# Optimization experiments

Hardware: AMD Instinct MI355X
Metric: run time of the kernel (lower is better)

Reference implementation:

```python
import jax, jax.numpy as jnp
import numpy as np

N_STATE = 16
PNAMES = ['in_w', 'conv_w', 'conv_b', 'xproj_w', 'dt_w', 'dt_b', 'A_log', 'D', 'ln_g', 'ln_b', 'out_w']


def _ss2d_params(key, dm, K):
    di = 2 * dm                       # expand = 2
    dr = (dm + 15) // 16              # dt_rank = ceil(d_model/16)
    ks = jax.random.split(key, 6)
    s = lambda k, shape, sc: jax.random.normal(k, shape, jnp.float32) * sc
    cshape = (di, 1, 3, 3) if K == 4 else (di, 1, 3)   # depthwise conv kernel
    return {
        'in_w': s(ks[0], (2 * di, dm), dm ** -0.5),
        'conv_w': s(ks[1], cshape, 0.3),
        'conv_b': jnp.zeros((di,), jnp.float32),
        'xproj_w': s(ks[2], (K, dr + 2 * N_STATE, di), di ** -0.5),
        'dt_w': s(ks[3], (K, di, dr), dr ** -0.5),
        'dt_b': s(ks[4], (K, di), 0.1),
        'A_log': jnp.log(jnp.arange(1, N_STATE + 1, dtype=jnp.float32)) * jnp.ones((K, di, N_STATE), jnp.float32),
        'D': jnp.ones((K, di), jnp.float32),
        'ln_g': jnp.ones((di,), jnp.float32),
        'ln_b': jnp.zeros((di,), jnp.float32),
        'out_w': s(ks[5], (dm, di), di ** -0.5),
    }


def _ln(x, g, b, eps=1e-5):
    m = jnp.mean(x, -1, keepdims=True)
    v = jnp.mean((x - m) ** 2, -1, keepdims=True)
    return (x - m) * jax.lax.rsqrt(v + eps) * g + b


def _scan_branches(xs, p):
    # xs: (B, K, di, L) -- selective scan along L for each direction k
    dr = p['dt_w'].shape[-1]
    x_dbl = jnp.einsum('bkdl,kcd->bkcl', xs, p['xproj_w'])
    dts, Bs, Cs = jnp.split(x_dbl, [dr, dr + N_STATE], axis=2)
    delta = jax.nn.softplus(jnp.einsum('bkrl,kdr->bkdl', dts, p['dt_w']) + p['dt_b'][None, :, :, None])
    A = -jnp.exp(p['A_log'])                               # (K, di, N)
    dA = jnp.exp(jnp.einsum('bkdl,kdn->lbkdn', delta, A))  # time-major for scan
    dBu = jnp.einsum('bkdl,bknl,bkdl->lbkdn', delta, Bs, xs)

    def step(h, io):
        a, bu = io
        h = a * h + bu
        return h, h

    h0 = jnp.zeros(dA.shape[1:], xs.dtype)
    _, hs = jax.lax.scan(step, h0, (dA, dBu))              # (L, B, K, di, N)
    y = jnp.einsum('lbkdn,bknl->bkdl', hs, Cs)
    return y + xs * p['D'][None, :, :, None]


def _ss2d_2d(x, p):
    # VMamba SS2D: x (B, H, W, dm) -> (B, H, W, dm), 4 scan directions
    xz = jnp.einsum('bhwc,ec->bhwe', x, p['in_w'])
    xin, z = jnp.split(xz, 2, -1)
    u = xin.transpose(0, 3, 1, 2)
    u = jax.lax.conv_general_dilated(u, p['conv_w'], (1, 1), 'SAME',
        dimension_numbers=('NCHW', 'OIHW', 'NCHW'), feature_group_count=u.shape[1])
    u = jax.nn.silu(u + p['conv_b'][None, :, None, None])
    Bb, di, H, W = u.shape
    L = H * W
    xf = u.reshape(Bb, di, L)                              # row-major
    xt = u.transpose(0, 1, 3, 2).reshape(Bb, di, L)        # col-major
    xs = jnp.stack([xf, xt, xf[..., ::-1], xt[..., ::-1]], 1)
    ys = _scan_branches(xs, p)                             # (B, 4, di, L)
    y0 = ys[:, 0]
    y2 = ys[:, 2][..., ::-1]
    y1 = ys[:, 1].reshape(Bb, di, W, H).transpose(0, 1, 3, 2).reshape(Bb, di, L)
    y3 = ys[:, 3][..., ::-1].reshape(Bb, di, W, H).transpose(0, 1, 3, 2).reshape(Bb, di, L)
    y = (y0 + y1 + y2 + y3).transpose(0, 2, 1).reshape(Bb, H, W, di)
    y = _ln(y, p['ln_g'], p['ln_b']) * jax.nn.silu(z)
    return jnp.einsum('bhwe,ce->bhwc', y, p['out_w'])


def _ss2d_1d(x, p):
    # SS2D_xb fuse block: x (B, L, dm) -> (B, L, dm), bidirectional 1D scan
    xz = jnp.einsum('blc,ec->ble', x, p['in_w'])
    xin, z = jnp.split(xz, 2, -1)
    u = xin.transpose(0, 2, 1)
    u = jax.lax.conv_general_dilated(u, p['conv_w'], (1,), 'SAME',
        dimension_numbers=('NCH', 'OIH', 'NCH'), feature_group_count=u.shape[1])
    u = jax.nn.silu(u + p['conv_b'][None, :, None])
    xs = jnp.stack([u, u[..., ::-1]], 1)                   # K = 2
    ys = _scan_branches(xs, p)
    y = (ys[:, 0] + ys[:, 1][..., ::-1]).transpose(0, 2, 1)
    y = _ln(y, p['ln_g'], p['ln_b']) * jax.nn.silu(z)
    return jnp.einsum('ble,ce->blc', y, p['out_w'])


def _bridge(C1, C2, C3, p1, p2, p3, pf, n1_g, n1_b):
    y1 = _ss2d_2d(C1.transpose(0, 2, 3, 1), p1).transpose(0, 3, 1, 2)
    y2 = _ss2d_2d(C2.transpose(0, 2, 3, 1), p2).transpose(0, 3, 1, 2)
    y3 = _ss2d_2d(C3.transpose(0, 2, 3, 1), p3).transpose(0, 3, 1, 2)
    B_, C, H, W = y1.shape                                 # C=24, H=W=112
    # faithful RAW reshapes (no permute), exactly as the torch source does
    F1 = y1.reshape(B_, H * W, C)
    F2 = y2.reshape(B_, H * W // 2, C)
    F3 = y3.reshape(B_, H * W // 4, C)
    F = jnp.concatenate([F1, F2, F3], axis=1)              # (B, 21952, 24)
    F = F + _ss2d_1d(_ln(F, n1_g, n1_b), pf)               # dropout = identity (eval)
    o1 = F[:, :12544, :].reshape(B_, C, H, W)
    o2 = F[:, 12544:18816, :].reshape(B_, C * 2, H // 2, W // 2)
    o3 = F[:, 18816:, :].reshape(B_, C * 4, H // 4, W // 4)
    return (o1, o2, o3)


def setup_inputs() -> dict:
    key = jax.random.key(0)
    ks = jax.random.split(key, 7)
    inp = {
        'C1': jax.random.normal(ks[0], (1, 24, 112, 112), jnp.float32),
        'C2': jax.random.normal(ks[1], (1, 48, 56, 56), jnp.float32),
        'C3': jax.random.normal(ks[2], (1, 96, 28, 28), jnp.float32),
    }
    for pfx, dm, K, kk in [('m1', 24, 4, ks[3]), ('m2', 48, 4, ks[4]), ('m3', 96, 4, ks[5]), ('fz', 24, 2, ks[6])]:
        p = _ss2d_params(kk, dm, K)
        for n in PNAMES:
            inp[pfx + '_' + n] = p[n]
    inp['n1_g'] = jnp.ones((24,), jnp.float32)
    inp['n1_b'] = jnp.zeros((24,), jnp.float32)
    return inp


def reference(C1, C2, C3, m1_in_w, m1_conv_w, m1_conv_b, m1_xproj_w, m1_dt_w, m1_dt_b, m1_A_log, m1_D, m1_ln_g, m1_ln_b, m1_out_w, m2_in_w, m2_conv_w, m2_conv_b, m2_xproj_w, m2_dt_w, m2_dt_b, m2_A_log, m2_D, m2_ln_g, m2_ln_b, m2_out_w, m3_in_w, m3_conv_w, m3_conv_b, m3_xproj_w, m3_dt_w, m3_dt_b, m3_A_log, m3_D, m3_ln_g, m3_ln_b, m3_out_w, fz_in_w, fz_conv_w, fz_conv_b, fz_xproj_w, fz_dt_w, fz_dt_b, fz_A_log, fz_D, fz_ln_g, fz_ln_b, fz_out_w, n1_g, n1_b):
    p1 = dict(zip(PNAMES, (m1_in_w, m1_conv_w, m1_conv_b, m1_xproj_w, m1_dt_w, m1_dt_b, m1_A_log, m1_D, m1_ln_g, m1_ln_b, m1_out_w)))
    p2 = dict(zip(PNAMES, (m2_in_w, m2_conv_w, m2_conv_b, m2_xproj_w, m2_dt_w, m2_dt_b, m2_A_log, m2_D, m2_ln_g, m2_ln_b, m2_out_w)))
    p3 = dict(zip(PNAMES, (m3_in_w, m3_conv_w, m3_conv_b, m3_xproj_w, m3_dt_w, m3_dt_b, m3_A_log, m3_D, m3_ln_g, m3_ln_b, m3_out_w)))
    pf = dict(zip(PNAMES, (fz_in_w, fz_conv_w, fz_conv_b, fz_xproj_w, fz_dt_w, fz_dt_b, fz_A_log, fz_D, fz_ln_g, fz_ln_b, fz_out_w)))
    return _bridge(C1, C2, C3, p1, p2, p3, pf, n1_g, n1_b)
```

## Files before the change

kernel.cpp:

```cpp
#include <hip/hip_runtime.h>
#include <hip/hip_bf16.h>
#include <hip/hip_fp16.h>

#define NST 16
#define L2E 1.4426950408889634f

typedef const void* inp;
typedef __half h16;

struct Job {
  inp Cin;
  inp in_w, conv_w, conv_b, xproj_w, dt_w, dt_b, A_log, D, ln_g, ln_b, out_w;
  h16 *u_pre, *z, *u, *delta, *Bs, *Cs, *yg;
  h16 *Hc;
  float *yacc, *Wc, *bc, *Ssum, *A2t, *F0out;
  float *outF; const float* resid;
  const int* aflg;
  int dm, di, dr, K, H, W, L, NCH, CLEN, is2d, TL, CG, PT, cinf;
};
struct Jobs { Job j[4]; int n; const int* dtf; };

__device__ __forceinline__ float ldw(inp p, size_t i, int f32){
  return f32 ? ((const float*)p)[i]
             : __bfloat162float(((const __hip_bfloat16*)p)[i]);
}
__device__ __forceinline__ float hf(const h16* p, size_t i){ return __half2float(p[i]); }
__device__ __forceinline__ float sigm(float x){ return 1.0f/(1.0f + __expf(-x)); }
__device__ __forceinline__ float silu_(float x){ return x * sigm(x); }
__device__ __forceinline__ float softp(float x){ return (x > 20.0f) ? x : __logf(1.0f + __expf(x)); }

__device__ __forceinline__ int map_pos(const Job& J, int k, int l){
  int rev   = J.is2d ? (k >= 2) : (k == 1);
  int trans = J.is2d ? (k & 1) : 0;
  int sl = rev ? (J.L - 1 - l) : l;
  return trans ? ((sl % J.H)*J.W + sl / J.H) : sl;
}

union F4H { float4 f; __half2 h[4]; };

__device__ __forceinline__ void ld16v(const h16* p, float* o){
  const float4* q = (const float4*)p;
  F4H a, b; a.f = q[0]; b.f = q[1];
  #pragma unroll
  for (int i = 0; i < 4; i++){ float2 x = __half22float2(a.h[i]); o[2*i] = x.x; o[2*i+1] = x.y; }
  #pragma unroll
  for (int i = 0; i < 4; i++){ float2 x = __half22float2(b.h[i]); o[8+2*i] = x.x; o[8+2*i+1] = x.y; }
}

__device__ __forceinline__ void ld8v(const h16* p, float* o){
  F4H a; a.f = *(const float4*)p;
  #pragma unroll
  for (int i = 0; i < 4; i++){ float2 x = __half22float2(a.h[i]); o[2*i] = x.x; o[2*i+1] = x.y; }
}

__device__ __forceinline__ void cvt16(float4 a4, float4 b4, float* o){
  F4H a, b; a.f = a4; b.f = b4;
  #pragma unroll
  for (int i = 0; i < 4; i++){ float2 x = __half22float2(a.h[i]); o[2*i] = x.x; o[2*i+1] = x.y; }
  #pragma unroll
  for (int i = 0; i < 4; i++){ float2 x = __half22float2(b.h[i]); o[8+2*i] = x.x; o[8+2*i+1] = x.y; }
}


__global__ void k_detect(const unsigned* D1, int* flag, int* afl){
  if (blockIdx.x == 0){
    if (threadIdx.x == 0) flag[0] = (D1[0] == 0x3F800000u) ? 1 : 0;
    if (threadIdx.x < 4) afl[threadIdx.x] = 1;
  }
}

__global__ void k_wcomb(Jobs js){
  int f32 = *js.dtf;
  int b = blockIdx.x;
  for (int m = 0; m < js.n; m++){
    const Job& J = js.j[m];
    int CC = J.di + 2*NST;
    int CC2 = CC + NST;
    int tot = J.K * CC2 * J.di;
    int nb = (tot + 255) >> 8;
    if (b < nb){
      int t = (b << 8) + (int)threadIdx.x;
      if (t < tot){
        int d = t % J.di; int r = t / J.di; int cout = r % CC2; int k = r / CC2;
        if (cout < J.di){
          float v = 0.0f;
          for (int rr = 0; rr < J.dr; rr++)
            v += ldw(J.dt_w, (size_t)(k*J.di + cout)*J.dr + rr, f32) *
                 ldw(J.xproj_w, (size_t)(k*(J.dr + 2*NST) + rr)*J.di + d, f32);
          J.Wc[(size_t)(k*CC + cout)*J.di + d] = v;
          if (d == 0) J.bc[k*CC + cout] = ldw(J.dt_b, k*J.di + cout, f32);
        } else if (cout < CC){
          int nn = cout - J.di;
          J.Wc[(size_t)(k*CC + cout)*J.di + d] =
            ldw(J.xproj_w, (size_t)(k*(J.dr + 2*NST) + J.dr + nn)*J.di + d, f32);
          if (d == 0) J.bc[k*CC + cout] = 0.0f;
        } else {
          int nn = cout - CC;
          float v = -L2E*__expf(ldw(J.A_log, ((size_t)(k*J.di + d) << 4) + nn, f32));
          J.A2t[(size_t)(k*NST + nn)*J.di + d] = v;
          float base = -L2E*__expf(ldw(J.A_log, ((size_t)(k*J.di + d) << 4), f32));
          float expect = (float)(nn+1)*base;
          if (fabsf(v - expect) > 1e-4f*fabsf(expect) + 1e-6f)
            atomicAnd((int*)J.aflg, 0);
        }
      }
      return;
    }
    b -= nb;
  }
}

__global__ void k_inproj(Jobs js){
  int f32 = *js.dtf;
  int b = blockIdx.x;
  for (int m = 0; m < js.n; m++){
    const Job& J = js.j[m];
    int tot = 2*J.di*J.L;
    int nb = (tot + 255) >> 8;
    if (b < nb){
      int cf = J.cinf ? 1 : f32;
      int t = (b << 8) + (int)threadIdx.x;
      if (t < tot){
        int p = t % J.L; int e = t / J.L;
        float acc;
        if (cf && f32){
          const float* Ci = (const float*)J.Cin;
          const float4* w4 = (const float4*)((const float*)J.in_w + (size_t)e*J.dm);
          float a0 = 0.f, a1 = 0.f, a2 = 0.f, a3 = 0.f;
          int n4 = J.dm >> 2;
          for (int c4 = 0; c4 < n4; c4++){
            float4 w = w4[c4];
            int c = c4 << 2;
            a0 = fmaf(Ci[(size_t)(c+0)*J.L + p], w.x, a0);
            a1 = fmaf(Ci[(size_t)(c+1)*J.L + p], w.y, a1);
            a2 = fmaf(Ci[(size_t)(c+2)*J.L + p], w.z, a2);
            a3 = fmaf(Ci[(size_t)(c+3)*J.L + p], w.w, a3);
          }
          acc = (a0+a1)+(a2+a3);
        } else {
          float a0 = 0.f, a1 = 0.f, a2 = 0.f, a3 = 0.f;
          for (int c = 0; c < J.dm; c += 4){
            a0 = fmaf(ldw(J.Cin, (size_t)(c+0)*J.L + p, cf), ldw(J.in_w, (size_t)e*J.dm + c+0, f32), a0);
            a1 = fmaf(ldw(J.Cin, (size_t)(c+1)*J.L + p, cf), ldw(J.in_w, (size_t)e*J.dm + c+1, f32), a1);
            a2 = fmaf(ldw(J.Cin, (size_t)(c+2)*J.L + p, cf), ldw(J.in_w, (size_t)e*J.dm + c+2, f32), a2);
            a3 = fmaf(ldw(J.Cin, (size_t)(c+3)*J.L + p, cf), ldw(J.in_w, (size_t)e*J.dm + c+3, f32), a3);
          }
          acc = (a0+a1)+(a2+a3);
        }
        if (e < J.di) J.u_pre[(size_t)p*J.di + e] = __float2half(acc);
        else          J.z[(size_t)p*J.di + (e - J.di)] = __float2half(acc);
      }
      return;
    }
    b -= nb;
  }
}

__global__ __launch_bounds__(256) void k_lnproj(const float* F0, inp g, inp bb, inp in_w,
                                                h16* u_pre, h16* z, int L, const int* dtf){
  __shared__ float xr[64][25];
  __shared__ float wsmT[24*96];
  int f32 = *dtf;
  int p0 = blockIdx.x << 6;
  int rows = L - p0; if (rows > 64) rows = 64;
  for (int i = threadIdx.x; i < 24*96; i += 256){
    int c = i / 96, e = i % 96;
    wsmT[i] = ldw(in_w, (size_t)e*24 + c, f32);
  }
  for (int idx = threadIdx.x; idx < rows*24; idx += 256){
    int r = idx / 24, c = idx % 24;
    xr[r][c] = F0[(size_t)(p0 + r)*24 + c];
  }
  __syncthreads();
  if ((int)threadIdx.x < rows){
    float* row = xr[threadIdx.x];
    float s = 0.f;
    #pragma unroll
    for (int c = 0; c < 24; c++) s += row[c];
    float mean = s * (1.0f/24.0f);
    float s2 = 0.f;
    #pragma unroll
    for (int c = 0; c < 24; c++){ float t = row[c]-mean; s2 = fmaf(t,t,s2); }
    float rs = rsqrtf(s2*(1.0f/24.0f) + 1e-5f);
    #pragma unroll
    for (int c = 0; c < 24; c++)
      row[c] = (row[c]-mean)*rs*ldw(g,c,f32) + ldw(bb,c,f32);
  }
  __syncthreads();
  for (int idx = threadIdx.x; idx < rows*96; idx += 256){
    int r = idx / 96, e = idx % 96;
    const float* row = xr[r];
    float acc = 0.f;
    #pragma unroll
    for (int c = 0; c < 24; c++) acc = fmaf(row[c], wsmT[c*96 + e], acc);
    if (e < 48) u_pre[(size_t)(p0+r)*48 + e] = __float2half(acc);
    else        z[(size_t)(p0+r)*48 + (e-48)] = __float2half(acc);
  }
}

__global__ void k_conv(Jobs js){
  int f32 = *js.dtf;
  int b = blockIdx.x;
  for (int m = 0; m < js.n; m++){
    const Job& J = js.j[m];
    int tot = J.L * J.di;
    int nb = (tot + 255) >> 8;
    if (b < nb){
      int t = (b << 8) + (int)threadIdx.x;
      if (t < tot){
        int d = t % J.di; int p = t / J.di;
        float acc = ldw(J.conv_b, d, f32);
        if (J.is2d){
          int h = p / J.W, w = p % J.W;
          for (int kh = 0; kh < 3; kh++){
            int hh = h + kh - 1;
            if ((unsigned)hh < (unsigned)J.H){
              for (int kw = 0; kw < 3; kw++){
                int ww = w + kw - 1;
                if ((unsigned)ww < (unsigned)J.W)
                  acc += ldw(J.conv_w, d*9 + kh*3 + kw, f32) * hf(J.u_pre, (size_t)(hh*J.W + ww)*J.di + d);
              }
            }
          }
        } else {
          for (int kk = 0; kk < 3; kk++){
            int pp = p + kk - 1;
            if ((unsigned)pp < (unsigned)J.L)
              acc += ldw(J.conv_w, d*3 + kk, f32) * hf(J.u_pre, (size_t)pp*J.di + d);
          }
        }
        J.u[(size_t)p*J.di + d] = __float2half(silu_(acc));
      }
      return;
    }
    b -= nb;
  }
}

__global__ void k_deltaBC(Jobs js){
  extern __shared__ float xt[];
  int b = blockIdx.x;
  for (int m = 0; m < js.n; m++){
    const Job& J = js.j[m];
    int TL = J.TL;
    int ntile = (J.L + TL - 1)/TL;
    int nb = J.K * ntile;
    if (b < nb){
      int k = b / ntile, tile = b % ntile;
      int l0 = tile * TL;
      int stride = J.di + 4;
      int CC = J.di + 2*NST;
      h16* yout = (h16*)(xt + (size_t)TL*stride);
      int d8n = J.di >> 3;
      int VE = TL * d8n;
      for (int idx = threadIdx.x; idx < VE; idx += 256){
        int ll = idx / d8n, d8 = idx % d8n;
        int l = l0 + ll;
        float o[8];
        if (l < J.L){
          ld8v(J.u + (size_t)map_pos(J, k, l)*J.di + (d8 << 3), o);
        } else {
          for (int i = 0; i < 8; i++) o[i] = 0.0f;
        }
        float4* dst = (float4*)(xt + ll*stride + (d8 << 3));
        dst[0] = make_float4(o[0],o[1],o[2],o[3]);
        dst[1] = make_float4(o[4],o[5],o[6],o[7]);
      }
      __syncthreads();
      int c4n = CC >> 2;
      int NL4 = TL >> 2;
      int items = NL4 * c4n;
      int n4 = J.di >> 2;
      for (int item = threadIdx.x; item < items; item += 256){
        int l4 = item % NL4;
        int cbase = (item / NL4) << 2;
        const float4* w0 = (const float4*)(J.Wc + (size_t)(k*CC + cbase+0)*J.di);
        const float4* w1 = (const float4*)(J.Wc + (size_t)(k*CC + cbase+1)*J.di);
        const float4* w2 = (const float4*)(J.Wc + (size_t)(k*CC + cbase+2)*J.di);
        const float4* w3 = (const float4*)(J.Wc + (size_t)(k*CC + cbase+3)*J.di);
        const float4* x0 = (const float4*)(xt + (l4 + 0*NL4)*stride);
        const float4* x1 = (const float4*)(xt + (l4 + 1*NL4)*stride);
        const float4* x2 = (const float4*)(xt + (l4 + 2*NL4)*stride);
        const float4* x3 = (const float4*)(xt + (l4 + 3*NL4)*stride);
        float acc[4][4];
        #pragma unroll
        for (int j = 0; j < 4; j++){
          acc[j][0]=0.f; acc[j][1]=0.f; acc[j][2]=0.f; acc[j][3]=0.f;
        }
        #pragma unroll 4
        for (int d4 = 0; d4 < n4; d4++){
          float4 W0 = w0[d4], W1 = w1[d4], W2 = w2[d4], W3 = w3[d4];
          float4 X0 = x0[d4], X1 = x1[d4], X2 = x2[d4], X3 = x3[d4];
          #define DOT4(a,X,W) { a = fmaf(X.x,W.x,a); a = fmaf(X.y,W.y,a); a = fmaf(X.z,W.z,a); a = fmaf(X.w,W.w,a); }
          DOT4(acc[0][0],X0,W0) DOT4(acc[0][1],X0,W1) DOT4(acc[0][2],X0,W2) DOT4(acc[0][3],X0,W3)
          DOT4(acc[1][0],X1,W0) DOT4(acc[1][1],X1,W1) DOT4(acc[1][2],X1,W2) DOT4(acc[1][3],X1,W3)
          DOT4(acc[2][0],X2,W0) DOT4(acc[2][1],X2,W1) DOT4(acc[2][2],X2,W2) DOT4(acc[2][3],X2,W3)
          DOT4(acc[3][0],X3,W0) DOT4(acc[3][1],X3,W1) DOT4(acc[3][2],X3,W2) DOT4(acc[3][3],X3,W3)
          #undef DOT4
        }
        float b0 = J.bc[k*CC + cbase+0], b1 = J.bc[k*CC + cbase+1];
        float b2 = J.bc[k*CC + cbase+2], b3 = J.bc[k*CC + cbase+3];
        int dosp = (cbase < J.di);
        #pragma unroll
        for (int j = 0; j < 4; j++){
          int ll = l4 + NL4*j;
          float av[4] = {acc[j][0]+b0, acc[j][1]+b1, acc[j][2]+b2, acc[j][3]+b3};
          h16* yo = yout + ll*CC + cbase;
          #pragma unroll
          for (int i = 0; i < 4; i++)
            yo[i] = __float2half(dosp ? softp(av[i]) : av[i]);
        }
      }
      __syncthreads();
      int WI = TL * c4n;
      for (int idx = threadIdx.x; idx < WI; idx += 256){
        int ll = idx / c4n, c4 = idx % c4n;
        int l = l0 + ll;
        if (l >= J.L) continue;
        int cbase = c4 << 2;
        uint2 v = *(const uint2*)(yout + ll*CC + cbase);
        if (cbase < J.di)
          *(uint2*)(J.delta + ((size_t)k*J.L + l)*J.di + cbase) = v;
        else if (cbase < J.di + NST)
          *(uint2*)(J.Bs + ((size_t)k*J.L + l)*NST + (cbase - J.di)) = v;
        else
          *(uint2*)(J.Cs + ((size_t)k*J.L + l)*NST + (cbase - J.di - NST)) = v;
      }
      return;
    }
    b -= nb;
  }
}

#define STEPRQ { if (rev){ if(--rm < 0){ rm = J.H - 1; qd--; } } else { if(++rm == J.H){ rm = 0; qd++; } } }

#define HUPD_GEN(S, DX, B) { \
  _Pragma("unroll") \
  for (int n = 0; n < NST; n++) h[n] = fmaf(exp2f((S) * A2[n]), h[n], (DX) * (B)[n]); }
#define HUPDY_GEN(S, DX, B, C, Y) { \
  _Pragma("unroll") \
  for (int n = 0; n < NST; n++){ h[n] = fmaf(exp2f((S) * A2[n]), h[n], (DX) * (B)[n]); (Y) = fmaf(h[n], (C)[n], (Y)); } }

#define POWTREE(Q, P) \
  float P[NST]; \
  P[0]=(Q); P[1]=P[0]*P[0]; P[2]=P[1]*P[0]; P[3]=P[1]*P[1]; \
  P[4]=P[3]*P[0]; P[5]=P[3]*P[1]; P[6]=P[3]*P[2]; P[7]=P[3]*P[3]; \
  P[8]=P[7]*P[0]; P[9]=P[7]*P[1]; P[10]=P[7]*P[2]; P[11]=P[7]*P[3]; \
  P[12]=P[7]*P[4]; P[13]=P[7]*P[5]; P[14]=P[7]*P[6]; P[15]=P[7]*P[7];

#define HUPD_POW(S, DX, B) { \
  float q_ = exp2f((S) * A0); \
  POWTREE(q_, Pw) \
  _Pragma("unroll") \
  for (int n = 0; n < NST; n++) h[n] = fmaf(Pw[n], h[n], (DX) * (B)[n]); }
#define HUPDY_POW(S, DX, B, C, Y) { \
  float q_ = exp2f((S) * A0); \
  POWTREE(q_, Pw) \
  _Pragma("unroll") \
  for (int n = 0; n < NST; n++){ h[n] = fmaf(Pw[n], h[n], (DX) * (B)[n]); (Y) = fmaf(h[n], (C)[n], (Y)); } }

__global__ __launch_bounds__(256) void k_passA(Jobs js){
  int b = blockIdx.x;
  int wid = (int)threadIdx.x >> 6;
  int lane = (int)threadIdx.x & 63;
  for (int m = 0; m < js.n; m++){
    const Job& J = js.j[m];
    int DG = (J.di + 63) >> 6;
    int units = J.K * J.NCH * DG;
    int nb = (units + 3) >> 2;
    if (b < nb){
      int uu = (b << 2) + wid;
      if (uu >= units) return;
      int afl = *J.aflg;
      int k = uu / (J.NCH * DG);
      int r = uu % (J.NCH * DG);
      int chunk = r / DG, dg = r % DG;
      int d = (dg << 6) + lane;
      if (d >= J.di) return;
      int c0 = chunk * J.CLEN;
      int c1 = c0 + J.CLEN; if (c1 > J.L) c1 = J.L;
      size_t sb = (size_t)(k*J.NCH + chunk);
      if (c0 >= J.L){
        J.Ssum[sb*J.di + d] = 0.0f;
        #pragma unroll
        for (int n = 0; n < NST; n++) J.Hc[(sb*NST + n)*J.di + d] = __float2half(0.0f);
        return;
      }
      float h[NST];
      #pragma unroll
      for (int n = 0; n < NST; n++) h[n] = 0.0f;
      float ss = 0.0f;
      int rev   = J.is2d ? (k >= 2) : (k == 1);
      int trans = J.is2d ? (k & 1) : 0;
      int rm = 0, qd = 0;
      if (trans){
        int sl0 = rev ? (J.L - 1 - c0) : c0;
        qd = sl0 / J.H; rm = sl0 % J.H;
      }
      const h16* dlt = J.delta + ((size_t)k*J.L)*J.di + d;
      const h16* Bb  = J.Bs + ((size_t)k*J.L)*NST;
      if (afl){
        float A0 = J.A2t[(size_t)(k*NST)*J.di + d];
        int l = c0;
        int pos0;
        h16 s0h, s1h, x0h, x1h;
        float4 B0a, B0b, B1a, B1b;
        if (trans){ pos0 = rm*J.W + qd; STEPRQ; } else pos0 = rev ? (J.L-1-l) : l;
        s0h = dlt[(size_t)l*J.di];
        x0h = J.u[(size_t)pos0*J.di + d];
        { const float4* bp = (const float4*)(Bb + (size_t)l*NST); B0a = bp[0]; B0b = bp[1]; }
        s1h = s0h; x1h = x0h; B1a = B0a; B1b = B0b;
        if (l + 1 < c1){
          int pos1;
          if (trans){ pos1 = rm*J.W + qd; STEPRQ; } else pos1 = rev ? (J.L-2-l) : (l+1);
          s1h = dlt[(size_t)(l+1)*J.di];
          x1h = J.u[(size_t)pos1*J.di + d];
          const float4* bq = (const float4*)(Bb + (size_t)(l+1)*NST); B1a = bq[0]; B1b = bq[1];
        }
        while (l < c1){
          int ln = l + 2;
          h16 ns0 = s0h, ns1 = s1h, nx0 = x0h, nx1 = x1h;
          float4 nB0a = B0a, nB0b = B0b, nB1a = B1a, nB1b = B1b;
          if (ln < c1){
            int np0;
            if (trans){ np0 = rm*J.W + qd; STEPRQ; } else np0 = rev ? (J.L-1-ln) : ln;
            ns0 = dlt[(size_t)ln*J.di];
            nx0 = J.u[(size_t)np0*J.di + d];
            const float4* bp = (const float4*)(Bb + (size_t)ln*NST); nB0a = bp[0]; nB0b = bp[1];
            if (ln + 1 < c1){
              int np1;
              if (trans){ np1 = rm*J.W + qd; STEPRQ; } else np1 = rev ? (J.L-2-ln) : (ln+1);
              ns1 = dlt[(size_t)(ln+1)*J.di];
              nx1 = J.u[(size_t)np1*J.di + d];
              const float4* bq = (const float4*)(Bb + (size_t)(ln+1)*NST); nB1a = bq[0]; nB1b = bq[1];
            }
          }
          {
            float s0 = __half2float(s0h), x0 = __half2float(x0h);
            float B0[NST]; cvt16(B0a, B0b, B0);
            float dx0 = s0 * x0; ss += s0;
            HUPD_POW(s0, dx0, B0)
            if (l + 1 < c1){
              float s1 = __half2float(s1h), x1 = __half2float(x1h);
              float B1[NST]; cvt16(B1a, B1b, B1);
              float dx1 = s1 * x1; ss += s1;
              HUPD_POW(s1, dx1, B1)
            }
          }
          l = ln;
          s0h = ns0; s1h = ns1; x0h = nx0; x1h = nx1;
          B0a = nB0a; B0b = nB0b; B1a = nB1a; B1b = nB1b;
        }
      } else {
        float A2[NST];
        #pragma unroll
        for (int n = 0; n < NST; n++) A2[n] = J.A2t[(size_t)(k*NST + n)*J.di + d];
        for (int l = c0; l < c1; l++){
          int pos;
          if (trans){ pos = rm*J.W + qd; STEPRQ; } else pos = rev ? (J.L-1-l) : l;
          float s0 = hf(dlt, (size_t)l*J.di);
          float x0 = hf(J.u, (size_t)pos*J.di + d);
          float B0[NST]; ld16v(Bb + (size_t)l*NST, B0);
          float dx0 = s0 * x0; ss += s0;
          HUPD_GEN(s0, dx0, B0)
        }
      }
      J.Ssum[sb*J.di + d] = ss;
      #pragma unroll
      for (int n = 0; n < NST; n++)
        J.Hc[(sb*NST + n)*J.di + d] = __float2half(h[n]);
      return;
    }
    b -= nb;
  }
}

__global__ __launch_bounds__(1024) void k_passB(Jobs js){
  __shared__ float sA[64*17], sH[64*17];
  int b = blockIdx.x;
  int sid = (int)threadIdx.x >> 4;
  int dd  = (int)threadIdx.x & 15;
  for (int m = 0; m < js.n; m++){
    const Job& J = js.j[m];
    int DT = J.di >> 4;
    int nb = J.K * NST * DT;
    if (b < nb){
      int k  = b / (NST*DT);
      int r  = b % (NST*DT);
      int n  = r / DT;
      int dt = r % DT;
      int d = dt*16 + dd;
      int SL = J.NCH >> 6;
      int c0 = sid*SL, c1 = c0 + SL;
      float An = J.A2t[(size_t)(k*NST + n)*J.di + d];
      float a = 1.0f, hagg = 0.0f;
      {
        size_t rb = (size_t)(k*J.NCH + c0);
        float ss = J.Ssum[rb*J.di + d];
        h16 hch  = J.Hc[(rb*NST + n)*J.di + d];
        for (int c = c0; c < c1; c++){
          float ssc = ss; h16 hcc = hch;
          if (c + 1 < c1){
            size_t rn = (size_t)(k*J.NCH + c + 1);
            ss  = J.Ssum[rn*J.di + d];
            hch = J.Hc[(rn*NST + n)*J.di + d];
          }
          float P = exp2f(An * ssc);
          hagg = fmaf(P, hagg, __half2float(hcc));
          a *= P;
        }
      }
      sA[sid*17+dd] = a; sH[sid*17+dd] = hagg;
      __syncthreads();
      #pragma unroll
      for (int s = 1; s < 64; s <<= 1){
        float pa = 1.0f, ph = 0.0f;
        if (sid >= s){ pa = sA[(sid-s)*17+dd]; ph = sH[(sid-s)*17+dd]; }
        __syncthreads();
        hagg = fmaf(a, ph, hagg);
        a *= pa;
        sA[sid*17+dd] = a; sH[sid*17+dd] = hagg;
        __syncthreads();
      }
      float Hp = (sid == 0) ? 0.0f : sH[(sid-1)*17+dd];
      {
        size_t rb = (size_t)(k*J.NCH + c0);
        float ss = J.Ssum[rb*J.di + d];
        h16 hch  = J.Hc[(rb*NST + n)*J.di + d];
        for (int c = c0; c < c1; c++){
          float ssc = ss; float hc = __half2float(hch);
          size_t idx = ((size_t)(k*J.NCH + c)*NST + n)*J.di + d;
          if (c + 1 < c1){
            size_t rn = (size_t)(k*J.NCH + c + 1);
            ss  = J.Ssum[rn*J.di + d];
            hch = J.Hc[(rn*NST + n)*J.di + d];
          }
          float P = exp2f(An * ssc);
          J.Hc[idx] = __float2half(Hp);
          Hp = fmaf(P, Hp, hc);
        }
      }
      return;
    }
    b -= nb;
  }
}

__global__ __launch_bounds__(256) void k_passC(Jobs js){
  int f32 = *js.dtf;
  int b = blockIdx.x;
  int wid = (int)threadIdx.x >> 6;
  int lane = (int)threadIdx.x & 63;
  for (int m = 0; m < js.n; m++){
    const Job& J = js.j[m];
    int DG = (J.di + 63) >> 6;
    int units = J.K * J.NCH * DG;
    int nb = (units + 3) >> 2;
    if (b < nb){
      int uu = (b << 2) + wid;
      if (uu >= units) return;
      int afl = *J.aflg;
      int k = uu / (J.NCH * DG);
      int r = uu % (J.NCH * DG);
      int chunk = r / DG, dg = r % DG;
      int d = (dg << 6) + lane;
      if (d >= J.di) return;
      int c0 = chunk * J.CLEN;
      int c1 = c0 + J.CLEN; if (c1 > J.L) c1 = J.L;
      if (c0 >= J.L) return;
      float h[NST];
      size_t sb = (size_t)(k*J.NCH + chunk);
      #pragma unroll
      for (int n = 0; n < NST; n++) h[n] = hf(J.Hc, (sb*NST + n)*J.di + d);
      float Dd = ldw(J.D, k*J.di + d, f32);
      float* yk = J.yacc + (size_t)k*J.L*J.di;
      int rev   = J.is2d ? (k >= 2) : (k == 1);
      int trans = J.is2d ? (k & 1) : 0;
      int rm = 0, qd = 0;
      if (trans){
        int sl0 = rev ? (J.L - 1 - c0) : c0;
        qd = sl0 / J.H; rm = sl0 % J.H;
      }
      const h16* dlt = J.delta + ((size_t)k*J.L)*J.di + d;
      const h16* Bb  = J.Bs + ((size_t)k*J.L)*NST;
      const h16* Cb  = J.Cs + ((size_t)k*J.L)*NST;
      if (afl){
        float A0 = J.A2t[(size_t)(k*NST)*J.di + d];
        int l = c0;
        int pos0, pos1 = 0;
        h16 s0h, s1h, x0h, x1h;
        float4 B0a, B0b, B1a, B1b, C0a, C0b, C1a, C1b;
        if (trans){ pos0 = rm*J.W + qd; STEPRQ; } else pos0 = rev ? (J.L-1-l) : l;
        s0h = dlt[(size_t)l*J.di];
        x0h = J.u[(size_t)pos0*J.di + d];
        { const float4* bp = (const float4*)(Bb + (size_t)l*NST); B0a = bp[0]; B0b = bp[1];
          const float4* cp = (const float4*)(Cb + (size_t)l*NST); C0a = cp[0]; C0b = cp[1]; }
        s1h = s0h; x1h = x0h; B1a = B0a; B1b = B0b; C1a = C0a; C1b = C0b;
        if (l + 1 < c1){
          if (trans){ pos1 = rm*J.W + qd; STEPRQ; } else pos1 = rev ? (J.L-2-l) : (l+1);
          s1h = dlt[(size_t)(l+1)*J.di];
          x1h = J.u[(size_t)pos1*J.di + d];
          const float4* bq = (const float4*)(Bb + (size_t)(l+1)*NST); B1a = bq[0]; B1b = bq[1];
          const float4* cq = (const float4*)(Cb + (size_t)(l+1)*NST); C1a = cq[0]; C1b = cq[1];
        }
        while (l < c1){
          int ln = l + 2;
          int np0 = pos0, np1 = pos1;
          h16 ns0 = s0h, ns1 = s1h, nx0 = x0h, nx1 = x1h;
          float4 nB0a = B0a, nB0b = B0b, nB1a = B1a, nB1b = B1b;
          float4 nC0a = C0a, nC0b = C0b, nC1a = C1a, nC1b = C1b;
          if (ln < c1){
            if (trans){ np0 = rm*J.W + qd; STEPRQ; } else np0 = rev ? (J.L-1-ln) : ln;
            ns0 = dlt[(size_t)ln*J.di];
            nx0 = J.u[(size_t)np0*J.di + d];
            { const float4* bp = (const float4*)(Bb + (size_t)ln*NST); nB0a = bp[0]; nB0b = bp[1];
              const float4* cp = (const float4*)(Cb + (size_t)ln*NST); nC0a = cp[0]; nC0b = cp[1]; }
            if (ln + 1 < c1){
              if (trans){ np1 = rm*J.W + qd; STEPRQ; } else np1 = rev ? (J.L-2-ln) : (ln+1);
              ns1 = dlt[(size_t)(ln+1)*J.di];
              nx1 = J.u[(size_t)np1*J.di + d];
              const float4* bq = (const float4*)(Bb + (size_t)(ln+1)*NST); nB1a = bq[0]; nB1b = bq[1];
              const float4* cq = (const float4*)(Cb + (size_t)(ln+1)*NST); nC1a = cq[0]; nC1b = cq[1];
            }
          }
          {
            float s0 = __half2float(s0h), x0 = __half2float(x0h);
            float B0[NST], C0[NST]; cvt16(B0a, B0b, B0); cvt16(C0a, C0b, C0);
            float dx0 = s0 * x0;
            float y0 = 0.0f;
            HUPDY_POW(s0, dx0, B0, C0, y0)
            y0 = fmaf(Dd, x0, y0);
            yk[(size_t)pos0*J.di + d] = y0;
            if (l + 1 < c1){
              float s1 = __half2float(s1h), x1 = __half2float(x1h);
              float B1[NST], C1[NST]; cvt16(B1a, B1b, B1); cvt16(C1a, C1b, C1);
              float dx1 = s1 * x1;
              float y1 = 0.0f;
              HUPDY_POW(s1, dx1, B1, C1, y1)
              y1 = fmaf(Dd, x1, y1);
              yk[(size_t)pos1*J.di + d] = y1;
            }
          }
          l = ln; pos0 = np0; pos1 = np1;
          s0h = ns0; s1h = ns1; x0h = nx0; x1h = nx1;
          B0a = nB0a; B0b = nB0b; B1a = nB1a; B1b = nB1b;
          C0a = nC0a; C0b = nC0b; C1a = nC1a; C1b = nC1b;
        }
      } else {
        float A2[NST];
        #pragma unroll
        for (int n = 0; n < NST; n++) A2[n] = J.A2t[(size_t)(k*NST + n)*J.di + d];
        for (int l = c0; l < c1; l++){
          int pos;
          if (trans){ pos = rm*J.W + qd; STEPRQ; } else pos = rev ? (J.L-1-l) : l;
          float s0 = hf(dlt, (size_t)l*J.di);
          float x0 = hf(J.u, (size_t)pos*J.di + d);
          float B0[NST], C0[NST];
          ld16v(Bb + (size_t)l*NST, B0);
          ld16v(Cb + (size_t)l*NST, C0);
          float dx0 = s0 * x0;
          float y0 = 0.0f;
          HUPDY_GEN(s0, dx0, B0, C0, y0)
          y0 = fmaf(Dd, x0, y0);
          yk[(size_t)pos*J.di + d] = y0;
        }
      }
      return;
    }
    b -= nb;
  }
}

__global__ void k_merge(Jobs js){
  extern __shared__ float sm[];
  int f32 = *js.dtf;
  int b = blockIdx.x;
  for (int m = 0; m < js.n; m++){
    const Job& J = js.j[m];
    int nbk = (J.L + J.PT - 1)/J.PT;
    if (b < nbk){
      int di = J.di, PT = J.PT;
      int st = di + 1, st2 = di + 2;
      int p0 = b * PT;
      int rows = J.L - p0; if (rows > PT) rows = PT;
      float* ya = sm;
      h16*   zz = (h16*)(sm + (size_t)PT*st);
      float* mres = (float*)(zz + (size_t)PT*st2);
      float* owT = mres + 2*PT;
      size_t LD = (size_t)J.L*di;
      int tot = rows*di;
      for (int idx = threadIdx.x; idx < tot; idx += 256){
        int r = idx / di, d = idx % di;
        size_t pp = (size_t)p0*di + idx;
        float v = J.yacc[pp];
        for (int k = 1; k < J.K; k++) v += J.yacc[(size_t)k*LD + pp];
        ya[r*st + d] = v;
        zz[r*st2 + d] = J.z[pp];
      }
      if (J.outF){
        for (int idx = threadIdx.x; idx < J.dm*di; idx += 256){
          int c = idx / di, e = idx % di;
          owT[e*25 + c] = ldw(J.out_w, (size_t)c*di + e, f32);
        }
      }
      __syncthreads();
      int wid = (int)threadIdx.x >> 6, lane = (int)threadIdx.x & 63;
      for (int r = wid; r < rows; r += 4){
        float s = 0.0f, s2 = 0.0f;
        for (int d = lane; d < di; d += 64){
          float v = ya[r*st + d];
          s += v; s2 = fmaf(v, v, s2);
        }
        for (int o = 32; o > 0; o >>= 1){
          s  += __shfl_down(s, o);
          s2 += __shfl_down(s2, o);
        }
        if (lane == 0){
          float mean = s / di;
          float var = s2/di - mean*mean;
          mres[r] = mean;
          mres[PT + r] = rsqrtf(var + 1e-5f);
        }
      }
      __syncthreads();
      if (J.outF){
        {
          int r = (int)threadIdx.x & (PT - 1);
          int dgrp = (int)threadIdx.x / PT;
          int G = 256 / PT;
          if (r < rows){
            float mean = mres[r], rs = mres[PT + r];
            for (int d = dgrp; d < di; d += G){
              float ln = (ya[r*st + d] - mean)*rs*ldw(J.ln_g, d, f32) + ldw(J.ln_b, d, f32);
              ya[r*st + d] = ln * silu_(__half2float(zz[r*st2 + d]));
            }
          }
        }
        __syncthreads();
        for (int idx = threadIdx.x; idx < rows*J.dm; idx += 256){
          int r = idx / J.dm, c = idx % J.dm;
          const float* lr = ya + r*st;
          float acc = 0.0f;
          for (int e = 0; e < di; e += 8){
            #pragma unroll
            for (int j = 0; j < 8; j++)
              acc = fmaf(lr[e+j], owT[(e+j)*25 + c], acc);
          }
          size_t o = (size_t)(p0 + r)*J.dm + c;
          J.outF[o] = J.resid[o] + acc;
        }
      } else {
        int r = (int)threadIdx.x & (PT - 1);
        int dgrp = (int)threadIdx.x / PT;
        int G = 256 / PT;
        if (r < rows){
          float mean = mres[r], rs = mres[PT + r];
          int p = p0 + r;
          for (int d = dgrp; d < di; d += G){
            float ln = (ya[r*st + d] - mean)*rs*ldw(J.ln_g, d, f32) + ldw(J.ln_b, d, f32);
            J.yg[(size_t)d*J.L + p] = __float2half(ln * silu_(__half2float(zz[r*st2 + d])));
          }
        }
      }
      return;
    }
    b -= nbk;
  }
}

__global__ void k_outproj(Jobs js){
  int f32 = *js.dtf;
  int b = blockIdx.x;
  for (int m = 0; m < js.n; m++){
    const Job& J = js.j[m];
    int tot = J.dm * J.L;
    int nb = (tot + 255) >> 8;
    if (b < nb){
      int t = (b << 8) + (int)threadIdx.x;
      if (t < tot){
        int p = t % J.L; int c = t / J.L;
        float acc = 0.0f;
        for (int e = 0; e < J.di; e += 8){
          #pragma unroll
          for (int j = 0; j < 8; j++)
            acc = fmaf(hf(J.yg, (size_t)(e+j)*J.L + p),
                       ldw(J.out_w, (size_t)c*J.di + e + j, f32), acc);
        }
        J.F0out[(size_t)c*J.L + p] = acc;
      }
      return;
    }
    b -= nb;
  }
}

static inline int cdiv_i(int a, int b){ return (a + b - 1)/b; }

extern "C" void kernel_launch(void* const* d_in, const int* in_sizes, int n_in,
                              void* d_out, int out_size, void* d_ws, size_t ws_size,
                              hipStream_t stream){
  (void)in_sizes; (void)n_in; (void)out_size; (void)ws_size;
  char* base = (char*)d_ws;
  size_t off = 0;
  auto alloc = [&](size_t bytes)->char*{
    off = (off + 255) & ~(size_t)255;
    char* p = base + off; off += bytes; return p;
  };

  int*   dtf = (int*)alloc(4);
  int*   afl = (int*)alloc(4*4);
  float* F0  = (float*)alloc(526848u*4);
  float* Wc1 = (float*)alloc(4u*80*48*4);   float* bc1 = (float*)alloc(4u*80*4);
  float* Wc2 = (float*)alloc(4u*128*96*4);  float* bc2 = (float*)alloc(4u*128*4);
  float* Wc3 = (float*)alloc(4u*224*192*4); float* bc3 = (float*)alloc(4u*224*4);
  float* Wcf = (float*)alloc(2u*80*48*4);   float* bcf = (float*)alloc(2u*80*4);
  float* A21 = (float*)alloc(4u*NST*48*4);
  float* A22 = (float*)alloc(4u*NST*96*4);
  float* A23 = (float*)alloc(4u*NST*192*4);
  float* A2f = (float*)alloc(2u*NST*48*4);
  size_t regionA = off;

  auto fill = [&](Job& J, int pbase, inp Cin, int cinf,
                  int dm, int di, int dr, int K, int H, int W, int L,
                  int NCH, int CLEN, int is2d, int TL, int PT,
                  float* Wc, float* bc, float* A2t, float* F0out){
    J.Cin = Cin; J.cinf = cinf;
    J.in_w    = d_in[pbase+0];
    J.conv_w  = d_in[pbase+1];
    J.conv_b  = d_in[pbase+2];
    J.xproj_w = d_in[pbase+3];
    J.dt_w    = d_in[pbase+4];
    J.dt_b    = d_in[pbase+5];
    J.A_log   = d_in[pbase+6];
    J.D       = d_in[pbase+7];
    J.ln_g    = d_in[pbase+8];
    J.ln_b    = d_in[pbase+9];
    J.out_w   = d_in[pbase+10];
    size_t LD = (size_t)L*di;
    J.yacc  = (float*)alloc((size_t)K*LD*4);
    J.u_pre = (h16*)J.yacc;
    J.z     = (h16*)alloc(LD*2);
    J.u     = (h16*)alloc(LD*2);
    J.yg    = J.u;
    J.delta = (h16*)alloc((size_t)K*LD*2);
    J.Bs    = (h16*)alloc((size_t)K*L*NST*2);
    J.Cs    = (h16*)alloc((size_t)K*L*NST*2);
    J.Hc    = (h16*)alloc((size_t)K*NCH*NST*di*2);
    J.Ssum  = (float*)alloc((size_t)K*NCH*di*4);
    J.Wc = Wc; J.bc = bc; J.A2t = A2t; J.F0out = F0out;
    J.outF = nullptr; J.resid = nullptr;
    J.dm=dm; J.di=di; J.dr=dr; J.K=K; J.H=H; J.W=W; J.L=L; J.NCH=NCH; J.CLEN=CLEN;
    J.is2d=is2d; J.TL=TL; J.CG=256/TL; J.PT=PT;
  };

  Jobs js3; js3.n = 3; js3.dtf = dtf;
  fill(js3.j[0], 25, d_in[2], 0, 96, 192, 6, 4,  28,  28,   784,   64, 13, 1, 16, 16, Wc3, bc3, A23, F0 + 451584);
  fill(js3.j[1], 14, d_in[1], 0, 48,  96, 3, 4,  56,  56,  3136,  256, 13, 1, 32, 32, Wc2, bc2, A22, F0 + 301056);
  fill(js3.j[2],  3, d_in[0], 0, 24,  48, 2, 4, 112, 112, 12544, 1024, 13, 1, 64, 32, Wc1, bc1, A21, F0);
  js3.j[0].aflg = afl + 0;
  js3.j[1].aflg = afl + 1;
  js3.j[2].aflg = afl + 2;

  off = regionA;
  Jobs js1; js1.n = 1; js1.dtf = dtf;
  fill(js1.j[0], 36, nullptr, 1, 24, 48, 2, 2, 21952, 1, 21952, 2048, 11, 0, 64, 32, Wcf, bcf, A2f, nullptr);
  js1.j[0].aflg = afl + 3;
  js1.j[0].outF = (float*)d_out;
  js1.j[0].resid = F0;

  Jobs js4; js4.n = 4; js4.dtf = dtf;
  js4.j[0] = js3.j[0]; js4.j[1] = js3.j[1]; js4.j[2] = js3.j[2]; js4.j[3] = js1.j[0];

  auto grids = [&](const Jobs& js, int which)->int{
    int g = 0;
    for (int m = 0; m < js.n; m++){
      const Job& J = js.j[m];
      switch (which){
        case 0: g += cdiv_i(J.K*(J.di+3*NST)*J.di, 256); break;
        case 1: g += cdiv_i(2*J.di*J.L, 256); break;
        case 2: g += cdiv_i(J.L*J.di, 256); break;
        case 3: g += J.K * cdiv_i(J.L, J.TL); break;
        case 4: g += cdiv_i(J.K * J.NCH * cdiv_i(J.di, 64), 4); break;
        case 5: g += J.K * NST * (J.di >> 4); break;
        case 6: g += cdiv_i(J.L, J.PT); break;
        case 7: g += cdiv_i(J.dm*J.L, 256); break;
      }
    }
    return g;
  };
  auto shm_dbc = [&](const Jobs& js)->int{
    int s = 0;
    for (int m = 0; m < js.n; m++){
      const Job& J = js.j[m];
      int v = J.TL*(J.di+4)*4 + J.TL*(J.di+2*NST)*2;
      if (v > s) s = v;
    }
    return s;
  };
  auto shm_merge = [&](const Jobs& js)->int{
    int s = 0;
    for (int m = 0; m < js.n; m++){
      const Job& J = js.j[m];
      int v = J.PT*(J.di+1)*4 + J.PT*(J.di+2)*2 + 2*J.PT*4 + (J.outF ? 48*25*4 : 0);
      if (v > s) s = v;
    }
    return s;
  };

  k_detect <<<1, 64, 0, stream>>>((const unsigned*)d_in[10], dtf, afl);

  k_wcomb  <<<grids(js4,0), 256, 0, stream>>>(js4);
  k_inproj <<<grids(js3,1), 256, 0, stream>>>(js3);
  k_conv   <<<grids(js3,2), 256, 0, stream>>>(js3);
  k_deltaBC<<<grids(js3,3), 256, shm_dbc(js3), stream>>>(js3);
  k_passA  <<<grids(js3,4), 256, 0, stream>>>(js3);
  k_passB  <<<grids(js3,5), 1024, 0, stream>>>(js3);
  k_passC  <<<grids(js3,4), 256, 0, stream>>>(js3);
  k_merge  <<<grids(js3,6), 256, shm_merge(js3), stream>>>(js3);
  k_outproj<<<grids(js3,7), 256, 0, stream>>>(js3);

  k_lnproj <<<cdiv_i(21952,64), 256, 0, stream>>>(F0, d_in[47], d_in[48], d_in[36],
                                                  js1.j[0].u_pre, js1.j[0].z, 21952, dtf);
  k_conv   <<<grids(js1,2), 256, 0, stream>>>(js1);
  k_deltaBC<<<grids(js1,3), 256, shm_dbc(js1), stream>>>(js1);
  k_passA  <<<grids(js1,4), 256, 0, stream>>>(js1);
  k_passB  <<<grids(js1,5), 1024, 0, stream>>>(js1);
  k_passC  <<<grids(js1,4), 256, 0, stream>>>(js1);
  k_merge  <<<grids(js1,6), 256, shm_merge(js1), stream>>>(js1);
}
```

Before: 451.0 us.

## Fuse weight-prep with in-projection, fuse LN-projection with 1D conv, retune fusion chunks

Merges the weight-combination and in-projection kernels into a single launch, and fuses the fusion stage's LayerNorm+in-projection with the depthwise 1D conv using a one-row halo in shared memory. This drops the u_pre round trip through global memory and removes two kernel launches. It also changes the fusion job's chunk count and chunk length (2048/11 to 4096/6), which alters the scan's chunk-parallel schedule. The fused kernel recomputes halo rows and assumes L is a multiple of 64 (21952 = 343*64).

```diff
diff --git a/kernel.cpp b/kernel.cpp
--- a/kernel.cpp
+++ b/kernel.cpp
@@ -69,11 +69,11 @@
   }
 }
 
-__global__ void k_wcomb(Jobs js){
-  int f32 = *js.dtf;
+__global__ void k_prep(Jobs jsW, Jobs jsI){
+  int f32 = *jsW.dtf;
   int b = blockIdx.x;
-  for (int m = 0; m < js.n; m++){
-    const Job& J = js.j[m];
+  for (int m = 0; m < jsW.n; m++){
+    const Job& J = jsW.j[m];
     int CC = J.di + 2*NST;
     int CC2 = CC + NST;
     int tot = J.K * CC2 * J.di;
@@ -108,13 +108,8 @@
     }
     b -= nb;
   }
-}
-
-__global__ void k_inproj(Jobs js){
-  int f32 = *js.dtf;
-  int b = blockIdx.x;
-  for (int m = 0; m < js.n; m++){
-    const Job& J = js.j[m];
+  for (int m = 0; m < jsI.n; m++){
+    const Job& J = jsI.j[m];
     int tot = 2*J.di*J.L;
     int nb = (tot + 255) >> 8;
     if (b < nb){
@@ -156,23 +151,25 @@
   }
 }
 
-__global__ __launch_bounds__(256) void k_lnproj(const float* F0, inp g, inp bb, inp in_w,
-                                                h16* u_pre, h16* z, int L, const int* dtf){
-  __shared__ float xr[64][25];
+__global__ __launch_bounds__(256) void k_lnprojconv(const float* F0, inp g, inp bb, inp in_w,
+                                                    inp conv_w, inp conv_b,
+                                                    h16* u, h16* z, int L, const int* dtf){
+  __shared__ float xr[66][25];
   __shared__ float wsmT[24*96];
+  __shared__ h16 up[66][48];
   int f32 = *dtf;
   int p0 = blockIdx.x << 6;
-  int rows = L - p0; if (rows > 64) rows = 64;
   for (int i = threadIdx.x; i < 24*96; i += 256){
     int c = i / 96, e = i % 96;
     wsmT[i] = ldw(in_w, (size_t)e*24 + c, f32);
   }
-  for (int idx = threadIdx.x; idx < rows*24; idx += 256){
-    int r = idx / 24, c = idx % 24;
-    xr[r][c] = F0[(size_t)(p0 + r)*24 + c];
+  for (int idx = threadIdx.x; idx < 66*24; idx += 256){
+    int rr = idx / 24, c = idx % 24;
+    int p = p0 + rr - 1;
+    xr[rr][c] = (p >= 0 && p < L) ? F0[(size_t)p*24 + c] : 0.0f;
   }
   __syncthreads();
-  if ((int)threadIdx.x < rows){
+  if ((int)threadIdx.x < 66){
     float* row = xr[threadIdx.x];
     float s = 0.f;
     #pragma unroll
@@ -187,14 +184,33 @@
       row[c] = (row[c]-mean)*rs*ldw(g,c,f32) + ldw(bb,c,f32);
   }
   __syncthreads();
-  for (int idx = threadIdx.x; idx < rows*96; idx += 256){
-    int r = idx / 96, e = idx % 96;
-    const float* row = xr[r];
+  for (int idx = threadIdx.x; idx < 66*48; idx += 256){
+    int rr = idx / 48, e = idx % 48;
+    int p = p0 + rr - 1;
+    float acc = 0.f;
+    if (p >= 0 && p < L){
+      const float* row = xr[rr];
+      #pragma unroll
+      for (int c = 0; c < 24; c++) acc = fmaf(row[c], wsmT[c*96 + e], acc);
+    }
+    up[rr][e] = __float2half(acc);
+  }
+  for (int idx = threadIdx.x; idx < 64*48; idx += 256){
+    int r = idx / 48, e = idx % 48;
+    const float* row = xr[r+1];
     float acc = 0.f;
     #pragma unroll
-    for (int c = 0; c < 24; c++) acc = fmaf(row[c], wsmT[c*96 + e], acc);
-    if (e < 48) u_pre[(size_t)(p0+r)*48 + e] = __float2half(acc);
-    else        z[(size_t)(p0+r)*48 + (e-48)] = __float2half(acc);
+    for (int c = 0; c < 24; c++) acc = fmaf(row[c], wsmT[c*96 + 48 + e], acc);
+    z[(size_t)(p0+r)*48 + e] = __float2half(acc);
+  }
+  __syncthreads();
+  for (int idx = threadIdx.x; idx < 64*48; idx += 256){
+    int r = idx / 48, d = idx % 48;
+    float acc = ldw(conv_b, d, f32);
+    #pragma unroll
+    for (int kk = 0; kk < 3; kk++)
+      acc += ldw(conv_w, d*3 + kk, f32) * __half2float(up[r+kk][d]);
+    u[(size_t)(p0+r)*48 + d] = __float2half(silu_(acc));
   }
 }
 
@@ -863,7 +879,7 @@
 
   off = regionA;
   Jobs js1; js1.n = 1; js1.dtf = dtf;
-  fill(js1.j[0], 36, nullptr, 1, 24, 48, 2, 2, 21952, 1, 21952, 2048, 11, 0, 64, 32, Wcf, bcf, A2f, nullptr);
+  fill(js1.j[0], 36, nullptr, 1, 24, 48, 2, 2, 21952, 1, 21952, 4096, 6, 0, 64, 32, Wcf, bcf, A2f, nullptr);
   js1.j[0].aflg = afl + 3;
   js1.j[0].outF = (float*)d_out;
   js1.j[0].resid = F0;
@@ -909,8 +925,7 @@
 
   k_detect <<<1, 64, 0, stream>>>((const unsigned*)d_in[10], dtf, afl);
 
-  k_wcomb  <<<grids(js4,0), 256, 0, stream>>>(js4);
-  k_inproj <<<grids(js3,1), 256, 0, stream>>>(js3);
+  k_prep   <<<grids(js4,0) + grids(js3,1), 256, 0, stream>>>(js4, js3);
   k_conv   <<<grids(js3,2), 256, 0, stream>>>(js3);
   k_deltaBC<<<grids(js3,3), 256, shm_dbc(js3), stream>>>(js3);
   k_passA  <<<grids(js3,4), 256, 0, stream>>>(js3);
@@ -919,9 +934,9 @@
   k_merge  <<<grids(js3,6), 256, shm_merge(js3), stream>>>(js3);
   k_outproj<<<grids(js3,7), 256, 0, stream>>>(js3);
 
-  k_lnproj <<<cdiv_i(21952,64), 256, 0, stream>>>(F0, d_in[47], d_in[48], d_in[36],
-                                                  js1.j[0].u_pre, js1.j[0].z, 21952, dtf);
-  k_conv   <<<grids(js1,2), 256, 0, stream>>>(js1);
+  k_lnprojconv<<<cdiv_i(21952,64), 256, 0, stream>>>(F0, d_in[47], d_in[48], d_in[36],
+                                                     d_in[37], d_in[38],
+                                                     js1.j[0].u, js1.j[0].z, 21952, dtf);
   k_deltaBC<<<grids(js1,3), 256, shm_dbc(js1), stream>>>(js1);
   k_passA  <<<grids(js1,4), 256, 0, stream>>>(js1);
   k_passB  <<<grids(js1,5), 1024, 0, stream>>>(js1);
```

Result: slower. 483.6 us (+7.2%).
